# Optimization experiments

Hardware: AMD Instinct MI355X
Metric: run time of the kernel (lower is better)

The kernel has to match this reference:

```python
import jax, jax.numpy as jnp
import numpy as np

N_SRC = 100_000   # hetero[s].num_nodes
N_DST = 100_000   # hetero[d].num_nodes
E     = 800_000   # edge_index.size(1)
D_SRC = 256       # node_dims['src']
D_DST = 256       # node_dims['dst']
D_REL = 128       # d_rel


def setup_inputs() -> dict:
    key = jax.random.key(0)
    ks = jax.random.split(key, 6)
    x_src = jax.random.normal(ks[0], (N_SRC, D_SRC), jnp.float32)
    x_dst = jax.random.normal(ks[1], (N_DST, D_DST), jnp.float32)
    # nn.Linear(d_in, d_rel, bias=False) weights, stored transposed as [d_in, d_rel]
    W_src = jax.random.normal(ks[2], (D_SRC, D_REL), jnp.float32) / np.sqrt(D_SRC).astype(np.float32)
    W_dst = jax.random.normal(ks[3], (D_DST, D_REL), jnp.float32) / np.sqrt(D_DST).astype(np.float32)
    edge_src = jax.random.randint(ks[4], (E,), 0, N_SRC, jnp.int32)  # edge_index[0]
    edge_dst = jax.random.randint(ks[5], (E,), 0, N_DST, jnp.int32)  # edge_index[1]
    return {"x_src": x_src, "x_dst": x_dst, "W_src": W_src, "W_dst": W_dst,
            "edge_src": edge_src, "edge_dst": edge_dst}


def reference(x_src, x_dst, W_src, W_dst, edge_src, edge_dst):
    # Per-type linear projection (bias-free), as in self.proj[nt](feats)
    p_src = x_src @ W_src            # [N_src, d_rel]
    p_dst = x_dst @ W_dst            # projected per module, unused by this edge type
    del p_dst

    # Degree of each destination (A.sum(dim=1)), clamped to >= 1.
    deg = jax.ops.segment_sum(jnp.ones((E,), jnp.float32), edge_dst,
                              num_segments=N_DST)
    deg = jnp.maximum(deg, 1.0)      # [N_dst]

    # Degree-normalized SpMM: sum of source features per destination / deg.
    # (coalescing duplicate edges sums their unit values; segment_sum matches.)
    agg = jax.ops.segment_sum(p_src[edge_src], edge_dst,
                              num_segments=N_DST)            # [N_dst, d_rel]
    dst = agg / deg[:, None]

    # rel_embs[et] = {'dst': dst, 'src_in': x_proj[s], 'deg_dst': deg}
    return dst, p_src, deg
```

## Files before the change

kernel.cpp:

```cpp
#include <hip/hip_runtime.h>
#include <hip/hip_bf16.h>

#define D_SRC 256
#define D_REL 128

typedef __bf16 bf16x8 __attribute__((ext_vector_type(8)));
typedef float f32x4 __attribute__((ext_vector_type(4)));
typedef float f32x2 __attribute__((ext_vector_type(2)));

typedef const __attribute__((address_space(1))) void GASV;
typedef __attribute__((address_space(3))) void LASV;

__global__ __launch_bounds__(64) void prep_w_kernel(const float* __restrict__ W,
                                                    bf16x8* __restrict__ Wt,
                                                    int* __restrict__ deg_i, int ndeg) {
    int c = blockIdx.x;
    int ks = c >> 3, n = c & 7;
    int lane = threadIdx.x;
    int col = n * 16 + (lane & 15);
    int k0 = ks * 32 + (lane >> 4) * 8;
    bf16x8 v;
#pragma unroll
    for (int j = 0; j < 8; ++j) v[j] = (__bf16)W[(size_t)(k0 + j) * D_REL + col];
    Wt[c * 64 + lane] = v;
    for (int i = blockIdx.x * 64 + lane; i < ndeg; i += 64 * 64) deg_i[i] = 0;
}

__global__ __launch_bounds__(256, 4) void proj_count_kernel(
    const float* __restrict__ x, const f32x4* __restrict__ Wt,
    float* __restrict__ out_f32, unsigned short* __restrict__ out_bf, int M,
    const int* __restrict__ edge_dst, int* __restrict__ deg_i,
    int* __restrict__ pos_arr, int E, int ncb) {
    __shared__ float xlds[32 * 256];
    int tid = threadIdx.x;

    if (blockIdx.x < ncb) {
        int stride = ncb * 256;
        for (int e = blockIdx.x * 256 + tid; e < E; e += stride)
            pos_arr[e] = atomicAdd(&deg_i[edge_dst[e]], 1);
        return;
    }

    int bid = blockIdx.x - ncb;
    int wid = tid >> 6, lane = tid & 63;
    int r = lane & 15, kq = lane >> 4;
    int row0 = bid * 32;

#pragma unroll
    for (int j = 0; j < 8; ++j) {
        int rl = wid * 8 + j;
        int grow = min(row0 + rl, M - 1);
        const float* src = x + (size_t)grow * D_SRC + ((lane ^ j) << 2);
        __builtin_amdgcn_global_load_lds((GASV*)src, (LASV*)&xlds[rl * 256], 16, 0, 0);
    }

    f32x4 wfv[2][8];
#pragma unroll
    for (int s = 0; s < 2; ++s)
#pragma unroll
        for (int ks = 0; ks < 8; ++ks)
            wfv[s][ks] = Wt[(ks * 8 + wid * 2 + s) * 64 + lane];
#pragma unroll
    for (int s = 0; s < 2; ++s)
#pragma unroll
        for (int ks = 0; ks < 8; ++ks)
            asm volatile("" : "+v"(wfv[s][ks]));

    __syncthreads();

    f32x4 acc[2][2];
#pragma unroll
    for (int t = 0; t < 2; ++t)
#pragma unroll
        for (int s = 0; s < 2; ++s) acc[t][s] = (f32x4)(0.f);

    const f32x4* xl = (const f32x4*)xlds;
    int r8 = r & 7;
#pragma unroll
    for (int ks = 0; ks < 8; ++ks) {
        int q0 = ks * 8 + kq * 2;
#pragma unroll
        for (int t = 0; t < 2; ++t) {
            int rl = t * 16 + r;
            f32x4 a0 = xl[rl * 64 + (q0 ^ r8)];
            f32x4 a1 = xl[rl * 64 + ((q0 + 1) ^ r8)];
            bf16x8 xf;
            xf[0] = (__bf16)a0[0]; xf[1] = (__bf16)a0[1];
            xf[2] = (__bf16)a0[2]; xf[3] = (__bf16)a0[3];
            xf[4] = (__bf16)a1[0]; xf[5] = (__bf16)a1[1];
            xf[6] = (__bf16)a1[2]; xf[7] = (__bf16)a1[3];
            acc[t][0] = __builtin_amdgcn_mfma_f32_16x16x32_bf16(
                __builtin_bit_cast(bf16x8, wfv[0][ks]), xf, acc[t][0], 0, 0, 0);
            acc[t][1] = __builtin_amdgcn_mfma_f32_16x16x32_bf16(
                __builtin_bit_cast(bf16x8, wfv[1][ks]), xf, acc[t][1], 0, 0, 0);
        }
    }

    int col0 = wid * 32;
#pragma unroll
    for (int t = 0; t < 2; ++t) {
        int prow = row0 + t * 16 + r;
        if (prow < M) {
            size_t o0 = (size_t)prow * D_REL + col0 + kq * 4;
            __builtin_nontemporal_store(acc[t][0], (f32x4*)(out_f32 + o0));
            __builtin_nontemporal_store(acc[t][1], (f32x4*)(out_f32 + o0 + 16));
            ushort4 b0, b1;
            b0.x = __bfloat16_as_ushort(__float2bfloat16(acc[t][0][0]));
            b0.y = __bfloat16_as_ushort(__float2bfloat16(acc[t][0][1]));
            b0.z = __bfloat16_as_ushort(__float2bfloat16(acc[t][0][2]));
            b0.w = __bfloat16_as_ushort(__float2bfloat16(acc[t][0][3]));
            b1.x = __bfloat16_as_ushort(__float2bfloat16(acc[t][1][0]));
            b1.y = __bfloat16_as_ushort(__float2bfloat16(acc[t][1][1]));
            b1.z = __bfloat16_as_ushort(__float2bfloat16(acc[t][1][2]));
            b1.w = __bfloat16_as_ushort(__float2bfloat16(acc[t][1][3]));
            *(ushort4*)(out_bf + o0) = b0;
            *(ushort4*)(out_bf + o0 + 16) = b1;
        }
    }
}

__global__ __launch_bounds__(1024) void scan_blocks(
    const int* __restrict__ deg_i, int* __restrict__ incl,
    int* __restrict__ bsums, int n) {
    int i = blockIdx.x * 1024 + threadIdx.x;
    int v = (i < n) ? deg_i[i] : 0;
    int lane = threadIdx.x & 63;
    int wid = threadIdx.x >> 6;
    int x = v;
#pragma unroll
    for (int off = 1; off < 64; off <<= 1) {
        int y = __shfl_up(x, off, 64);
        if (lane >= off) x += y;
    }
    __shared__ int wsum[16];
    if (lane == 63) wsum[wid] = x;
    __syncthreads();
    if (wid == 0 && lane < 16) {
        int s = wsum[lane];
#pragma unroll
        for (int off = 1; off < 16; off <<= 1) {
            int y = __shfl_up(s, off, 64);
            if (lane >= off) s += y;
        }
        wsum[lane] = s;
    }
    __syncthreads();
    int add = (wid > 0) ? wsum[wid - 1] : 0;
    x += add;
    if (i < n) incl[i] = x;
    if (threadIdx.x == 1023) bsums[blockIdx.x] = x;
}

__global__ __launch_bounds__(1024) void finalize_kernel(
    const int* __restrict__ deg_i, const int* __restrict__ incl,
    const int* __restrict__ bsums, int* __restrict__ row_start,
    float* __restrict__ deg_out, int n, int E) {
    __shared__ int soff;
    int bid = blockIdx.x;
    if (threadIdx.x < 64) {
        int lane = threadIdx.x;
        int s = 0;
        for (int i = lane; i < bid; i += 64) s += bsums[i];
#pragma unroll
        for (int m = 32; m >= 1; m >>= 1) s += __shfl_xor(s, m, 64);
        if (lane == 0) soff = s;
    }
    __syncthreads();
    int off = soff;
    int i = bid * 1024 + threadIdx.x;
    if (i < n) {
        row_start[i] = off + incl[i] - deg_i[i];
        deg_out[i] = (float)max(deg_i[i], 1);
    }
    if (i == 0) row_start[n] = E;
}

__global__ void fill_kernel(const int* __restrict__ edge_src,
                            const int* __restrict__ edge_dst,
                            const int* __restrict__ row_start,
                            const int* __restrict__ pos_arr,
                            int* __restrict__ bucket, int E) {
    int e = blockIdx.x * 256 + threadIdx.x;
    if (e < E) {
        int d = edge_dst[e];
        bucket[row_start[d] + pos_arr[e]] = edge_src[e];
    }
}

__global__ __launch_bounds__(256) void gather_kernel(
    const unsigned int* __restrict__ p_bf, const int* __restrict__ row_start,
    const int* __restrict__ bucket, const float* __restrict__ deg_out,
    float* __restrict__ dst, int n) {
    int row = blockIdx.x * 4 + (threadIdx.x >> 6);
    int lane = threadIdx.x & 63;
    if (row >= n) return;
    int beg = row_start[row], end = row_start[row + 1];
    float ax = 0.f, ay = 0.f;
    int idx = beg;
    for (; idx + 8 <= end; idx += 8) {
        int s[8];
        unsigned int v[8];
#pragma unroll
        for (int u = 0; u < 8; ++u) s[u] = bucket[idx + u];
#pragma unroll
        for (int u = 0; u < 8; ++u) v[u] = p_bf[(size_t)s[u] * 64 + lane];
#pragma unroll
        for (int u = 0; u < 8; ++u) {
            ax += __uint_as_float(v[u] << 16);
            ay += __uint_as_float(v[u] & 0xffff0000u);
        }
    }
    for (; idx + 4 <= end; idx += 4) {
        int s0 = bucket[idx + 0], s1 = bucket[idx + 1];
        int s2 = bucket[idx + 2], s3 = bucket[idx + 3];
        unsigned int v0 = p_bf[(size_t)s0 * 64 + lane];
        unsigned int v1 = p_bf[(size_t)s1 * 64 + lane];
        unsigned int v2 = p_bf[(size_t)s2 * 64 + lane];
        unsigned int v3 = p_bf[(size_t)s3 * 64 + lane];
        ax += __uint_as_float(v0 << 16) + __uint_as_float(v1 << 16)
            + __uint_as_float(v2 << 16) + __uint_as_float(v3 << 16);
        ay += __uint_as_float(v0 & 0xffff0000u) + __uint_as_float(v1 & 0xffff0000u)
            + __uint_as_float(v2 & 0xffff0000u) + __uint_as_float(v3 & 0xffff0000u);
    }
    for (; idx < end; ++idx) {
        int s = bucket[idx];
        unsigned int v = p_bf[(size_t)s * 64 + lane];
        ax += __uint_as_float(v << 16);
        ay += __uint_as_float(v & 0xffff0000u);
    }
    float dinv = 1.0f / deg_out[row];
    f32x2 o;
    o[0] = ax * dinv;
    o[1] = ay * dinv;
    f32x2* dp = (f32x2*)dst + (size_t)row * 64 + lane;
    __builtin_nontemporal_store(o, dp);
}

extern "C" void kernel_launch(void* const* d_in, const int* in_sizes, int n_in,
                              void* d_out, int out_size, void* d_ws, size_t ws_size,
                              hipStream_t stream) {
    const float* x_src = (const float*)d_in[0];
    const float* W_src = (const float*)d_in[2];
    const int* edge_src = (const int*)d_in[4];
    const int* edge_dst = (const int*)d_in[5];

    const int N_SRC = in_sizes[0] / D_SRC;
    const int N_DST = in_sizes[1] / D_SRC;
    const int E = in_sizes[4];

    float* out_dst = (float*)d_out;
    float* out_psrc = out_dst + (size_t)N_DST * D_REL;
    float* out_deg = out_psrc + (size_t)N_SRC * D_REL;

    int* deg_i = (int*)d_ws;
    int* incl = deg_i + N_DST;
    int* row_start = incl + N_DST;
    int* bsums = row_start + N_DST + 1;
    int* pos_arr = bsums + 128;
    int* bucket = pos_arr + E;
    size_t int_bytes = (size_t)(3 * N_DST + 1 + 128 + 2 * (size_t)E) * sizeof(int);
    size_t wt_off = (int_bytes + 255) & ~(size_t)255;
    bf16x8* Wt = (bf16x8*)((char*)d_ws + wt_off);
    size_t pbf_off = wt_off + 65536;
    unsigned short* p_bf = (unsigned short*)((char*)d_ws + pbf_off);

    prep_w_kernel<<<64, 64, 0, stream>>>(W_src, Wt, deg_i, N_DST);
    {
        int nproj = (N_SRC + 31) / 32;
        int ncb = 512;
        proj_count_kernel<<<ncb + nproj, 256, 0, stream>>>(
            x_src, (const f32x4*)Wt, out_psrc, p_bf, N_SRC,
            edge_dst, deg_i, pos_arr, E, ncb);
    }
    int nb = (N_DST + 1023) / 1024;
    scan_blocks<<<nb, 1024, 0, stream>>>(deg_i, incl, bsums, N_DST);
    finalize_kernel<<<nb, 1024, 0, stream>>>(deg_i, incl, bsums, row_start, out_deg, N_DST, E);
    fill_kernel<<<(E + 255) / 256, 256, 0, stream>>>(edge_src, edge_dst, row_start, pos_arr, bucket, E);
    gather_kernel<<<(N_DST + 3) / 4, 256, 0, stream>>>(
        (const unsigned int*)p_bf, row_start, bucket, out_deg, out_dst, N_DST);
}
```

Before: 129.9 us.

## Split x fp32-to-bf16 conversion into separate pass before projection GEMM

The fp32 x_src is now converted to bf16 in its own elementwise kernel, merged with the degree-count atomics, and written to workspace. A separate GEMM kernel then loads bf16 rows into LDS with a new swizzle and feeds MFMA directly, with no per-element conversion in the inner loop. This adds a full extra write and read of x (about 51MB written plus 51MB read back) and an extra launch. In exchange the GEMM halves its LDS footprint and ALU conversion work.

After: 148.2 us. 1.14x slower.

```diff
diff --git a/kernel.cpp b/kernel.cpp
--- a/kernel.cpp
+++ b/kernel.cpp
@@ -26,32 +26,50 @@
     for (int i = blockIdx.x * 64 + lane; i < ndeg; i += 64 * 64) deg_i[i] = 0;
 }
 
-__global__ __launch_bounds__(256, 4) void proj_count_kernel(
-    const float* __restrict__ x, const f32x4* __restrict__ Wt,
-    float* __restrict__ out_f32, unsigned short* __restrict__ out_bf, int M,
+__global__ __launch_bounds__(256) void xcvt_count_kernel(
+    const f32x4* __restrict__ x4, uint4* __restrict__ xbf, int n8,
     const int* __restrict__ edge_dst, int* __restrict__ deg_i,
     int* __restrict__ pos_arr, int E, int ncb) {
-    __shared__ float xlds[32 * 256];
     int tid = threadIdx.x;
-
     if (blockIdx.x < ncb) {
         int stride = ncb * 256;
         for (int e = blockIdx.x * 256 + tid; e < E; e += stride)
             pos_arr[e] = atomicAdd(&deg_i[edge_dst[e]], 1);
         return;
     }
-
-    int bid = blockIdx.x - ncb;
+    int i = (blockIdx.x - ncb) * 256 + tid;
+    if (i >= n8) return;
+    f32x4 a = __builtin_nontemporal_load(x4 + 2 * (size_t)i);
+    f32x4 b = __builtin_nontemporal_load(x4 + 2 * (size_t)i + 1);
+    uint4 v;
+    v.x = (unsigned)__bfloat16_as_ushort(__float2bfloat16(a[0])) |
+          ((unsigned)__bfloat16_as_ushort(__float2bfloat16(a[1])) << 16);
+    v.y = (unsigned)__bfloat16_as_ushort(__float2bfloat16(a[2])) |
+          ((unsigned)__bfloat16_as_ushort(__float2bfloat16(a[3])) << 16);
+    v.z = (unsigned)__bfloat16_as_ushort(__float2bfloat16(b[0])) |
+          ((unsigned)__bfloat16_as_ushort(__float2bfloat16(b[1])) << 16);
+    v.w = (unsigned)__bfloat16_as_ushort(__float2bfloat16(b[2])) |
+          ((unsigned)__bfloat16_as_ushort(__float2bfloat16(b[3])) << 16);
+    xbf[i] = v;
+}
+
+__global__ __launch_bounds__(256, 4) void proj_gemm_kernel(
+    const unsigned short* __restrict__ xbf, const f32x4* __restrict__ Wt,
+    float* __restrict__ out_f32, unsigned short* __restrict__ out_bf, int M) {
+    __shared__ __align__(16) char xlds[32 * 512];
+    int tid = threadIdx.x;
     int wid = tid >> 6, lane = tid & 63;
     int r = lane & 15, kq = lane >> 4;
-    int row0 = bid * 32;
-
-#pragma unroll
-    for (int j = 0; j < 8; ++j) {
-        int rl = wid * 8 + j;
+    int row0 = blockIdx.x * 32;
+
+#pragma unroll
+    for (int j = 0; j < 4; ++j) {
+        int rl = wid * 8 + 2 * j + (lane >> 5);
         int grow = min(row0 + rl, M - 1);
-        const float* src = x + (size_t)grow * D_SRC + ((lane ^ j) << 2);
-        __builtin_amdgcn_global_load_lds((GASV*)src, (LASV*)&xlds[rl * 256], 16, 0, 0);
+        int sslot = (lane & 31) ^ ((rl & 7) << 1);
+        const char* src = (const char*)xbf + (size_t)grow * 512 + (sslot << 4);
+        __builtin_amdgcn_global_load_lds((GASV*)src,
+                                         (LASV*)&xlds[(wid * 8 + 2 * j) * 512], 16, 0, 0);
     }
 
     f32x4 wfv[2][8];
@@ -74,21 +92,14 @@
 #pragma unroll
         for (int s = 0; s < 2; ++s) acc[t][s] = (f32x4)(0.f);
 
-    const f32x4* xl = (const f32x4*)xlds;
-    int r8 = r & 7;
+    const bf16x8* xl = (const bf16x8*)xlds;
+    int sw = (r & 7) << 1;
 #pragma unroll
     for (int ks = 0; ks < 8; ++ks) {
-        int q0 = ks * 8 + kq * 2;
 #pragma unroll
         for (int t = 0; t < 2; ++t) {
             int rl = t * 16 + r;
-            f32x4 a0 = xl[rl * 64 + (q0 ^ r8)];
-            f32x4 a1 = xl[rl * 64 + ((q0 + 1) ^ r8)];
-            bf16x8 xf;
-            xf[0] = (__bf16)a0[0]; xf[1] = (__bf16)a0[1];
-            xf[2] = (__bf16)a0[2]; xf[3] = (__bf16)a0[3];
-            xf[4] = (__bf16)a1[0]; xf[5] = (__bf16)a1[1];
-            xf[6] = (__bf16)a1[2]; xf[7] = (__bf16)a1[3];
+            bf16x8 xf = xl[rl * 32 + ((ks * 4 + kq) ^ sw)];
             acc[t][0] = __builtin_amdgcn_mfma_f32_16x16x32_bf16(
                 __builtin_bit_cast(bf16x8, wfv[0][ks]), xf, acc[t][0], 0, 0, 0);
             acc[t][1] = __builtin_amdgcn_mfma_f32_16x16x32_bf16(
@@ -263,15 +274,19 @@
     bf16x8* Wt = (bf16x8*)((char*)d_ws + wt_off);
     size_t pbf_off = wt_off + 65536;
     unsigned short* p_bf = (unsigned short*)((char*)d_ws + pbf_off);
+    size_t xbf_off = (pbf_off + (size_t)N_SRC * D_REL * 2 + 255) & ~(size_t)255;
+    unsigned short* x_bf = (unsigned short*)((char*)d_ws + xbf_off);
 
     prep_w_kernel<<<64, 64, 0, stream>>>(W_src, Wt, deg_i, N_DST);
     {
-        int nproj = (N_SRC + 31) / 32;
+        int n8 = N_SRC * D_SRC / 8;
+        int ncvt = (n8 + 255) / 256;
         int ncb = 512;
-        proj_count_kernel<<<ncb + nproj, 256, 0, stream>>>(
-            x_src, (const f32x4*)Wt, out_psrc, p_bf, N_SRC,
-            edge_dst, deg_i, pos_arr, E, ncb);
-    }
+        xcvt_count_kernel<<<ncb + ncvt, 256, 0, stream>>>(
+            (const f32x4*)x_src, (uint4*)x_bf, n8, edge_dst, deg_i, pos_arr, E, ncb);
+    }
+    proj_gemm_kernel<<<(N_SRC + 31) / 32, 256, 0, stream>>>(
+        x_bf, (const f32x4*)Wt, out_psrc, p_bf, N_SRC);
     int nb = (N_DST + 1023) / 1024;
     scan_blocks<<<nb, 1024, 0, stream>>>(deg_i, incl, bsums, N_DST);
     finalize_kernel<<<nb, 1024, 0, stream>>>(deg_i, incl, bsums, row_start, out_deg, N_DST, E);
```
